# Kernel optimization log

Measured on AMD Instinct MI355X. Metric: run time of the kernel, lower is better.

Reference implementation:

```python
import jax, jax.numpy as jnp
import numpy as np

B, BS, M, D = 64, 8, 512, 256  # b = bs * neg_sample_num, neg_sample_num = 8
NEG_FILL = -1e10


def setup_inputs() -> dict:
    key = jax.random.key(0)
    ks = jax.random.split(key, 7)
    x = jax.random.normal(ks[0], (B, M, D), jnp.float32)
    y = jax.random.normal(ks[1], (BS, M, D), jnp.float32)
    mask_x = jax.random.randint(ks[2], (B, M), 0, 2).astype(bool).at[:, 0].set(True)
    mask_y = jax.random.randint(ks[3], (BS, M), 0, 2).astype(bool).at[:, 0].set(True)
    scale = 1.0 / np.sqrt(D)
    Wq = jax.random.normal(ks[4], (D, D), jnp.float32) * scale  # torch Linear weight [out,in]
    Wk = jax.random.normal(ks[5], (D, D), jnp.float32) * scale
    Wv = jax.random.normal(ks[6], (D, D), jnp.float32) * scale
    return {"x": x, "y": y, "mask_x": mask_x, "mask_y": mask_y, "Wq": Wq, "Wk": Wk, "Wv": Wv}


def reference(x, y, mask_x, mask_y, Wq, Wk, Wv):
    # Projections (torch Linear: x @ W.T, no bias)
    Qx, Kx, Vx = x @ Wq.T, x @ Wk.T, x @ Wv.T
    Qy, Ky, Vy = y @ Wq.T, y @ Wk.T, y @ Wv.T
    b, m, d = Qx.shape
    bs = Ky.shape[0]
    neg = b // bs  # neg_sample_num branch (bs != b)

    scores_x = jnp.einsum('bid,bjd->bij', Qx, Kx)   # [b,m,m]
    scores_y = jnp.einsum('bid,bjd->bij', Qy, Ky)   # [bs,m,m]
    # Q_x grouped as [bs, neg, m, d] then transposed to [neg, bs, m, d];
    # K_y is tiled over neg (pure broadcast), so contract directly against [bs,m,d].
    Qx_e = Qx.reshape(bs, neg, m, d).swapaxes(0, 1)  # [neg,bs,m,d]
    scores_xy = jnp.einsum('nsid,sjd->nsij', Qx_e, Ky)  # [neg,bs,m,m]

    mx = mask_x[:, :, None]  # [b,m,1]
    my = mask_y[:, :, None]  # [bs,m,1]
    scores_x = jnp.where(mx & mx.swapaxes(1, 2), scores_x, NEG_FILL)
    scores_y = jnp.where(my & my.swapaxes(1, 2), scores_y, NEG_FILL)

    mask_xy = mask_x.reshape(bs, neg, m, 1).swapaxes(0, 1) & mask_y[None, :, None, :]  # [neg,bs,m,m]
    scores_xy = jnp.where(mask_xy, scores_xy, NEG_FILL)

    # y_len[n, s] = sum(mask_y[s]) for every n (repeat/view/sum/transpose in torch)
    y_len = jnp.broadcast_to(jnp.sum(mask_y.astype(jnp.int32), axis=1)[None, :], (neg, bs))

    probs_x = jax.nn.softmax(scores_x, axis=-1)
    probs_y = jax.nn.softmax(scores_y, axis=-1)
    probs_xy = jax.nn.softmax(scores_xy, axis=-1)

    ctx_x = jnp.einsum('bij,bjd->bid', probs_x, Vx)
    ctx_y = jnp.einsum('bij,bjd->bid', probs_y, Vy)
    return (ctx_x, ctx_y, scores_x, scores_y, probs_xy, mask_xy, y_len)
```

## Files before the change

### kernel.cpp

```cpp
#include <hip/hip_runtime.h>
#include <cstdint>

#define NEG_FILL_F (-10000000000.0f)
constexpr int BB     = 64;
constexpr int BS_    = 8;
constexpr int MM     = 512;
constexpr int DD     = 256;
constexpr int ROWS_X = BB * MM;
constexpr int ROWS_Y = BS_ * MM;
constexpr int ROWS_ALL = ROWS_X + ROWS_Y;
constexpr int KS     = 512;

typedef __attribute__((ext_vector_type(8))) short short8;
typedef __attribute__((ext_vector_type(4))) float f32x4;

__device__ inline unsigned short rne_bf16(float f) {
    unsigned int u = __float_as_uint(f);
    u = (u + 0x7FFFu + ((u >> 16) & 1u)) >> 16;
    return (unsigned short)u;
}
__device__ inline float bf2f(unsigned short h) {
    return __uint_as_float(((unsigned int)h) << 16);
}

__device__ inline f32x4 mfma16(short8 a, short8 b, f32x4 c) {
    return __builtin_amdgcn_mfma_f32_16x16x32_bf16(a, b, c, 0, 0, 0);
}

__device__ inline void gld16(const unsigned short* g, unsigned short* l) {
    __builtin_amdgcn_global_load_lds(
        (const __attribute__((address_space(1))) unsigned int*)g,
        (__attribute__((address_space(3))) unsigned int*)l, 16, 0, 0);
}

__device__ inline int awin32(int w) { return (((w >> 3) == 1) ? 256 : 0) + (w & 7) * 32; }
__device__ inline int bwin32(int w) { return (((w >> 3) == 2) ? 256 : 0) + (w & 7) * 32; }

__device__ inline void stage32(unsigned short* dstbase,
                               const unsigned short* __restrict__ src,
                               int srccol, int wave, int lane)
{
    #pragma unroll
    for (int s4 = 0; s4 < 2; ++s4) {
        const int c   = s4 * 256 + wave * 64 + lane;
        const int r   = c >> 2;
        const int cin = (c & 3) ^ (r & 3);
        gld16(src + (size_t)r * KS + srccol + cin * 8,
              dstbase + (size_t)(s4 * 256 + wave * 64) * 8);
    }
}

__device__ inline void frag4_x32(const unsigned short (*T)[32], int rbase,
                                 int lid, int quad, short8 f[4])
{
    const int q = quad ^ (lid & 3);
    #pragma unroll
    for (int i = 0; i < 4; ++i)
        f[i] = *(const short8*)&T[rbase + i * 16 + lid][q * 8];
}

__global__ __launch_bounds__(256) void convw_kernel(
    const float* __restrict__ Wq, const float* __restrict__ Wk,
    const float* __restrict__ Wv, unsigned short* __restrict__ Wb)
{
    const int g  = blockIdx.x * 256 + threadIdx.x;
    const int e  = g * 8;
    const int zi = e >> 16;
    const int off = e & 65535;
    const int row = off >> 8, k0 = off & 255;
    const float* W = (zi == 0) ? Wq : (zi == 1 ? Wk : Wv);
    float4 v0 = *(const float4*)(W + off);
    float4 v1 = *(const float4*)(W + off + 4);
    const float fv[8] = {v0.x, v0.y, v0.z, v0.w, v1.x, v1.y, v1.z, v1.w};
    short8 hh, ll;
    #pragma unroll
    for (int i = 0; i < 8; ++i) {
        unsigned short h = rne_bf16(fv[i]);
        hh[i] = (short)h;
        ll[i] = (short)rne_bf16(fv[i] - bf2f(h));
    }
    unsigned short* dst = Wb + (size_t)zi * 131072 + (size_t)row * KS;
    *(short8*)(dst + k0)       = hh;
    *(short8*)(dst + 256 + k0) = ll;
}

__global__ __launch_bounds__(256) void convx_kernel(
    const float* __restrict__ x, const float* __restrict__ y,
    unsigned short* __restrict__ xs)
{
    const int g   = blockIdx.x * 256 + threadIdx.x;
    const int row = g >> 5;
    const int off = (g & 31) * 8;
    const float* src = (row < ROWS_X) ? (x + (size_t)row * DD)
                                      : (y + (size_t)(row - ROWS_X) * DD);
    float4 v0 = *(const float4*)(src + off);
    float4 v1 = *(const float4*)(src + off + 4);
    const float fv[8] = {v0.x, v0.y, v0.z, v0.w, v1.x, v1.y, v1.z, v1.w};
    short8 hh, ll;
    #pragma unroll
    for (int i = 0; i < 8; ++i) {
        unsigned short h = rne_bf16(fv[i]);
        hh[i] = (short)h;
        ll[i] = (short)rne_bf16(fv[i] - bf2f(h));
    }
    unsigned short* dst = xs + (size_t)row * KS;
    *(short8*)(dst + off)       = hh;
    *(short8*)(dst + 256 + off) = ll;
}

__global__ __launch_bounds__(256) void proj_kernel(
    const unsigned short* __restrict__ xs,
    const unsigned short* __restrict__ Wb,
    unsigned short* __restrict__ Qa, unsigned short* __restrict__ Kb,
    unsigned short* __restrict__ Vt)
{
    const int xcd = blockIdx.x & 7, idx = blockIdx.x >> 3;
    const int lin = xcd * 216 + idx;
    const int bx  = lin / 6;
    const int rem = lin - bx * 6;
    const int z    = rem >> 1;
    const int row0 = bx * 128;
    const int col0 = (rem & 1) * 128;
    const unsigned short* Asrc = xs + (size_t)row0 * KS;
    const unsigned short* Bsrc = Wb + (size_t)z * 131072 + (size_t)col0 * KS;

    __shared__ unsigned short Ab[2][128][32];
    __shared__ unsigned short Bb[2][128][32];

    const int t = threadIdx.x;
    const int wave = t >> 6, lane = t & 63, quad = lane >> 4, lid = lane & 15;
    const int wrow = (wave & 1) * 64, wcol = (wave >> 1) * 64;

    f32x4 acc[4][4];
    #pragma unroll
    for (int i = 0; i < 4; ++i)
        #pragma unroll
        for (int j = 0; j < 4; ++j) acc[i][j] = (f32x4){0.f, 0.f, 0.f, 0.f};

    stage32(&Ab[0][0][0], Asrc, awin32(0), wave, lane);
    stage32(&Bb[0][0][0], Bsrc, bwin32(0), wave, lane);
    __syncthreads();
    int cur = 0;
    for (int w = 0; w < 23; ++w) {
        stage32(&Ab[cur ^ 1][0][0], Asrc, awin32(w + 1), wave, lane);
        stage32(&Bb[cur ^ 1][0][0], Bsrc, bwin32(w + 1), wave, lane);
        short8 af[4], bf_[4];
        frag4_x32(Ab[cur], wrow, lid, quad, af);
        frag4_x32(Bb[cur], wcol, lid, quad, bf_);
        #pragma unroll
        for (int i = 0; i < 4; ++i)
            #pragma unroll
            for (int j = 0; j < 4; ++j)
                acc[i][j] = mfma16(af[i], bf_[j], acc[i][j]);
        __syncthreads();
        cur ^= 1;
    }
    {
        short8 af[4], bf_[4];
        frag4_x32(Ab[cur], wrow, lid, quad, af);
        frag4_x32(Bb[cur], wcol, lid, quad, bf_);
        #pragma unroll
        for (int i = 0; i < 4; ++i)
            #pragma unroll
            for (int j = 0; j < 4; ++j)
                acc[i][j] = mfma16(af[i], bf_[j], acc[i][j]);
    }

    if (z == 2) {
        #pragma unroll
        for (int i = 0; i < 4; ++i) {
            const int rg = row0 + wrow + i * 16 + quad * 4;
            const int b  = rg >> 9;
            const int j  = rg & 511;
            #pragma unroll
            for (int jt = 0; jt < 4; ++jt) {
                const int col = col0 + wcol + jt * 16 + lid;
                *(ushort4*)(Vt + (size_t)b * DD * MM + (size_t)col * MM + j) =
                    make_ushort4(rne_bf16(acc[i][jt][0]), rne_bf16(acc[i][jt][1]),
                                 rne_bf16(acc[i][jt][2]), rne_bf16(acc[i][jt][3]));
            }
        }
    } else {
        unsigned short* dst = (z == 0) ? Qa : Kb;
        #pragma unroll
        for (int i = 0; i < 4; ++i) {
            const int rg = row0 + wrow + i * 16 + quad * 4;
            #pragma unroll
            for (int r = 0; r < 4; ++r) {
                unsigned short* rowp = dst + (size_t)(rg + r) * KS;
                #pragma unroll
                for (int jt = 0; jt < 4; ++jt) {
                    const int col = col0 + wcol + jt * 16 + lid;
                    const float v = acc[i][jt][r];
                    unsigned short h = rne_bf16(v);
                    rowp[col]       = h;
                    rowp[256 + col] = rne_bf16(v - bf2f(h));
                }
            }
        }
    }
}

__global__ __launch_bounds__(256, 2) void scores_self_kernel(
    const unsigned short* __restrict__ Qa,
    const unsigned short* __restrict__ Kb,
    const int* __restrict__ mask_x, const int* __restrict__ mask_y,
    float* __restrict__ Sbase, unsigned short* __restrict__ P,
    float* __restrict__ inv_all)
{
    const int xcd = blockIdx.x & 7, idx = blockIdx.x >> 3;
    const int lin = xcd * 72 + idx;
    const int z    = lin >> 3;
    const int brow = (lin & 7) * 64;
    const unsigned short* Asrc = Qa + (size_t)(z * MM + brow) * KS;
    const unsigned short* Bsrc = Kb + (size_t)z * MM * KS;
    const int* msk = (z < 64) ? (mask_x + z * MM) : (mask_y + (z - 64) * MM);
    float* S = Sbase + (size_t)z * MM * MM;

    __shared__ unsigned short Ab[2][64][32];
    __shared__ unsigned short Bb[2][512][32];
    __shared__ float pm4[64][4], ps4[64][4], smx[64];

    const int t = threadIdx.x;
    const int wave = t >> 6, lane = t & 63, quad = lane >> 4, lid = lane & 15;
    const int wcol = wave * 128;

    f32x4 acc[4][8];
    #pragma unroll
    for (int i = 0; i < 4; ++i)
        #pragma unroll
        for (int j = 0; j < 8; ++j) acc[i][j] = (f32x4){0.f, 0.f, 0.f, 0.f};

    auto stage = [&](int buf, int w) {
        {
            const int r = t >> 2, cin = (t & 3) ^ (r & 3);
            gld16(Asrc + (size_t)r * KS + awin32(w) + cin * 8,
                  &Ab[buf][0][0] + (size_t)(wave * 64) * 8);
        }
        const int bw = bwin32(w);
        #pragma unroll
        for (int k = 0; k < 8; ++k) {
            const int c = k * 256 + t;
            const int r = c >> 2, cin = (c & 3) ^ (r & 3);
            gld16(Bsrc + (size_t)r * KS + bw + cin * 8,
                  &Bb[buf][0][0] + (size_t)(k * 256 + wave * 64) * 8);
        }
    };
    auto comp = [&](int buf) {
        short8 af[4], bv[8];
        frag4_x32(Ab[buf], 0, lid, quad, af);
        frag4_x32(Bb[buf], wcol, lid, quad, bv);
        frag4_x32(Bb[buf], wcol + 64, lid, quad, bv + 4);
        #pragma unroll
        for (int i = 0; i < 4; ++i)
            #pragma unroll
            for (int j = 0; j < 8; ++j)
                acc[i][j] = mfma16(af[i], bv[j], acc[i][j]);
    };

    stage(0, 0);
    __syncthreads();
    int cur = 0;
    for (int w = 0; w < 23; ++w) {
        stage(cur ^ 1, w + 1);
        comp(cur);
        __syncthreads();
        cur ^= 1;
    }
    comp(cur);

    int mcol[8];
    #pragma unroll
    for (int j = 0; j < 8; ++j) mcol[j] = msk[wcol + j * 16 + lid];

    #pragma unroll
    for (int i = 0; i < 4; ++i) {
        #pragma unroll
        for (int r = 0; r < 4; ++r) {
            const int rl = i * 16 + quad * 4 + r;
            const bool mr = (msk[brow + rl] != 0);
            float* Srow = S + (size_t)(brow + rl) * MM;
            float vv[8];
            float mt = -3.4e38f;
            #pragma unroll
            for (int j = 0; j < 8; ++j) {
                const int col = wcol + j * 16 + lid;
                const bool valid = mr && (mcol[j] != 0);
                vv[j] = valid ? acc[i][j][r] : NEG_FILL_F;
                Srow[col] = vv[j];
                mt = fmaxf(mt, vv[j]);
            }
            #pragma unroll
            for (int o = 1; o < 16; o <<= 1) mt = fmaxf(mt, __shfl_xor(mt, o));
            float se = 0.f;
            #pragma unroll
            for (int j = 0; j < 8; ++j) se += __expf(vv[j] - mt);
            #pragma unroll
            for (int o = 1; o < 16; o <<= 1) se += __shfl_xor(se, o);
            if (lid == 0) { pm4[rl][wave] = mt; ps4[rl][wave] = se; }
        }
    }
    __syncthreads();
    if (t < 64) {
        const float m = fmaxf(fmaxf(pm4[t][0], pm4[t][1]),
                              fmaxf(pm4[t][2], pm4[t][3]));
        float s = 0.f;
        #pragma unroll
        for (int c = 0; c < 4; ++c) s += ps4[t][c] * __expf(pm4[t][c] - m);
        smx[t] = m;
        inv_all[z * MM + brow + t] = 1.0f / s;
    }
    __syncthreads();
    #pragma unroll
    for (int i = 0; i < 4; ++i) {
        #pragma unroll
        for (int r = 0; r < 4; ++r) {
            const int rl = i * 16 + quad * 4 + r;
            const bool mr = (msk[brow + rl] != 0);
            const float m = smx[rl];
            unsigned short* Prow = P + (size_t)(z * MM + brow + rl) * KS;
            #pragma unroll
            for (int j = 0; j < 8; ++j) {
                const int col = wcol + j * 16 + lid;
                const bool valid = mr && (mcol[j] != 0);
                const float v = valid ? acc[i][j][r] : NEG_FILL_F;
                Prow[col] = rne_bf16(__expf(v - m));
            }
        }
    }
}

__global__ __launch_bounds__(256, 2) void scores_xy_kernel(
    const unsigned short* __restrict__ Qa, const unsigned short* __restrict__ Kb,
    const int* __restrict__ mask_x, const int* __restrict__ mask_y,
    float* __restrict__ Prb, float* __restrict__ Mb)
{
    const int xcd = blockIdx.x & 7, idx = blockIdx.x >> 3;
    const int lin = xcd * 64 + idx;
    const int zz = lin >> 3;
    const int brow = (lin & 7) * 64;
    const int s = zz >> 3, n = zz & 7;
    const int zo = n * 8 + s;
    const int bq = s * 8 + n;
    const int bk = s;
    const unsigned short* Asrc = Qa + (size_t)(bq * MM + brow) * KS;
    const unsigned short* Bsrc = Kb + (size_t)(ROWS_X + bk * MM) * KS;
    const int* mq = mask_x + bq * MM;
    const int* mk = mask_y + bk * MM;
    float* Pl = Prb + (size_t)zo * MM * MM;
    float* Ml = Mb  + (size_t)zo * MM * MM;

    __shared__ unsigned short Ab[2][64][32];
    __shared__ unsigned short Bb[2][512][32];
    __shared__ float pm4[64][4], ps4[64][4], smx[64], sin[64];

    const int t = threadIdx.x;
    const int wave = t >> 6, lane = t & 63, quad = lane >> 4, lid = lane & 15;
    const int wcol = wave * 128;

    f32x4 acc[4][8];
    #pragma unroll
    for (int i = 0; i < 4; ++i)
        #pragma unroll
        for (int j = 0; j < 8; ++j) acc[i][j] = (f32x4){0.f, 0.f, 0.f, 0.f};

    auto stage = [&](int buf, int w) {
        {
            const int r = t >> 2, cin = (t & 3) ^ (r & 3);
            gld16(Asrc + (size_t)r * KS + w * 32 + cin * 8,
                  &Ab[buf][0][0] + (size_t)(wave * 64) * 8);
        }
        #pragma unroll
        for (int k = 0; k < 8; ++k) {
            const int c = k * 256 + t;
            const int r = c >> 2, cin = (c & 3) ^ (r & 3);
            gld16(Bsrc + (size_t)r * KS + w * 32 + cin * 8,
                  &Bb[buf][0][0] + (size_t)(k * 256 + wave * 64) * 8);
        }
    };
    auto comp = [&](int buf) {
        short8 af[4], bv[8];
        frag4_x32(Ab[buf], 0, lid, quad, af);
        frag4_x32(Bb[buf], wcol, lid, quad, bv);
        frag4_x32(Bb[buf], wcol + 64, lid, quad, bv + 4);
        #pragma unroll
        for (int i = 0; i < 4; ++i)
            #pragma unroll
            for (int j = 0; j < 8; ++j)
                acc[i][j] = mfma16(af[i], bv[j], acc[i][j]);
    };

    stage(0, 0);
    __syncthreads();
    int cur = 0;
    for (int w = 0; w < 7; ++w) {
        stage(cur ^ 1, w + 1);
        comp(cur);
        __syncthreads();
        cur ^= 1;
    }
    comp(cur);

    int mcol[8];
    #pragma unroll
    for (int j = 0; j < 8; ++j) mcol[j] = mk[wcol + j * 16 + lid];

    #pragma unroll
    for (int i = 0; i < 4; ++i) {
        #pragma unroll
        for (int r = 0; r < 4; ++r) {
            const int rl = i * 16 + quad * 4 + r;
            const bool mr = (mq[brow + rl] != 0);
            float* Mrow = Ml + (size_t)(brow + rl) * MM;
            float vv[8];
            float mt = -3.4e38f;
            #pragma unroll
            for (int j = 0; j < 8; ++j) {
                const int col = wcol + j * 16 + lid;
                const bool valid = mr && (mcol[j] != 0);
                vv[j] = valid ? acc[i][j][r] : NEG_FILL_F;
                Mrow[col] = valid ? 1.0f : 0.0f;
                mt = fmaxf(mt, vv[j]);
            }
            #pragma unroll
            for (int o = 1; o < 16; o <<= 1) mt = fmaxf(mt, __shfl_xor(mt, o));
            float se = 0.f;
            #pragma unroll
            for (int j = 0; j < 8; ++j) se += __expf(vv[j] - mt);
            #pragma unroll
            for (int o = 1; o < 16; o <<= 1) se += __shfl_xor(se, o);
            if (lid == 0) { pm4[rl][wave] = mt; ps4[rl][wave] = se; }
        }
    }
    __syncthreads();
    if (t < 64) {
        const float m = fmaxf(fmaxf(pm4[t][0], pm4[t][1]),
                              fmaxf(pm4[t][2], pm4[t][3]));
        float ssum = 0.f;
        #pragma unroll
        for (int c = 0; c < 4; ++c) ssum += ps4[t][c] * __expf(pm4[t][c] - m);
        smx[t] = m;
        sin[t] = 1.0f / ssum;
    }
    __syncthreads();
    #pragma unroll
    for (int i = 0; i < 4; ++i) {
        #pragma unroll
        for (int r = 0; r < 4; ++r) {
            const int rl = i * 16 + quad * 4 + r;
            const bool mr = (mq[brow + rl] != 0);
            const float m = smx[rl], iv = sin[rl];
            float* Prow = Pl + (size_t)(brow + rl) * MM;
            #pragma unroll
            for (int j = 0; j < 8; ++j) {
                const int col = wcol + j * 16 + lid;
                const bool valid = mr && (mcol[j] != 0);
                const float v = valid ? acc[i][j][r] : NEG_FILL_F;
                Prow[col] = __expf(v - m) * iv;
            }
        }
    }
}

__global__ __launch_bounds__(256) void ctx_kernel(
    const unsigned short* __restrict__ P, const float* __restrict__ inv_all,
    const unsigned short* __restrict__ Vt_base, float* __restrict__ Obase)
{
    const int xcd = blockIdx.x & 7, idx = blockIdx.x >> 3;
    const int lin = xcd * 72 + idx;
    const int b    = lin >> 3;
    const int brow = (lin & 7) * 64;
    const unsigned short* Psrc = P + (size_t)(b * MM + brow) * KS;
    const unsigned short* Vt   = Vt_base + (size_t)b * DD * MM;
    float*                O    = Obase + (size_t)b * MM * DD;
    const float*          iv   = inv_all + b * MM + brow;

    __shared__ unsigned short Ab[2][64][32];
    __shared__ unsigned short Bb[2][256][32];

    const int t = threadIdx.x;
    const int wave = t >> 6, lane = t & 63, quad = lane >> 4, lid = lane & 15;
    const int wcol = wave * 64;

    f32x4 acc[4][4];
    #pragma unroll
    for (int i = 0; i < 4; ++i)
        #pragma unroll
        for (int j = 0; j < 4; ++j) acc[i][j] = (f32x4){0.f, 0.f, 0.f, 0.f};

    auto stage = [&](int buf, int w) {
        {
            const int r = t >> 2, cin = (t & 3) ^ (r & 3);
            gld16(Psrc + (size_t)r * KS + w * 32 + cin * 8,
                  &Ab[buf][0][0] + (size_t)(wave * 64) * 8);
        }
        #pragma unroll
        for (int k = 0; k < 4; ++k) {
            const int c = k * 256 + t;
            const int r = c >> 2, cin = (c & 3) ^ (r & 3);
            gld16(Vt + (size_t)r * MM + w * 32 + cin * 8,
                  &Bb[buf][0][0] + (size_t)(k * 256 + wave * 64) * 8);
        }
    };
    auto comp = [&](int buf) {
        short8 af[4], bf_[4];
        frag4_x32(Ab[buf], 0, lid, quad, af);
        frag4_x32(Bb[buf], wcol, lid, quad, bf_);
        #pragma unroll
        for (int i = 0; i < 4; ++i)
            #pragma unroll
            for (int j = 0; j < 4; ++j)
                acc[i][j] = mfma16(af[i], bf_[j], acc[i][j]);
    };

    stage(0, 0);
    __syncthreads();
    int cur = 0;
    for (int w = 0; w < 15; ++w) {
        stage(cur ^ 1, w + 1);
        comp(cur);
        __syncthreads();
        cur ^= 1;
    }
    comp(cur);

    #pragma unroll
    for (int i = 0; i < 4; ++i) {
        const int rl0 = i * 16 + quad * 4;
        float inv[4];
        #pragma unroll
        for (int r = 0; r < 4; ++r) inv[r] = iv[rl0 + r];
        #pragma unroll
        for (int jt = 0; jt < 4; ++jt) {
            const int col = wcol + jt * 16 + lid;
            #pragma unroll
            for (int r = 0; r < 4; ++r)
                O[(size_t)(brow + rl0 + r) * DD + col] = acc[i][jt][r] * inv[r];
        }
    }
}

__global__ void ylen_kernel(const int* __restrict__ mask_y, float* __restrict__ out)
{
    const int s = blockIdx.x;
    const int lane = threadIdx.x;
    int c = 0;
    #pragma unroll
    for (int k = 0; k < 8; ++k) c += (mask_y[s * MM + k * 64 + lane] != 0);
    #pragma unroll
    for (int off = 32; off; off >>= 1) c += __shfl_xor(c, off);
    if (lane < 8) out[lane * 8 + s] = (float)c;
}

extern "C" void kernel_launch(void* const* d_in, const int* in_sizes, int n_in,
                              void* d_out, int out_size, void* d_ws, size_t ws_size,
                              hipStream_t stream)
{
    const float* x      = (const float*)d_in[0];
    const float* y      = (const float*)d_in[1];
    const int*   mask_x = (const int*)d_in[2];
    const int*   mask_y = (const int*)d_in[3];
    const float* Wq     = (const float*)d_in[4];
    const float* Wk     = (const float*)d_in[5];
    const float* Wv     = (const float*)d_in[6];
    float* out = (float*)d_out;

    unsigned short* Wb = (unsigned short*)d_ws;
    unsigned short* xs = Wb + 393216;
    unsigned short* Qa = xs + 18874368;
    unsigned short* Kb = Qa + 18874368;
    unsigned short* Vt = Kb + 18874368;
    float* inv_all = (float*)(Vt + 9437184);

    float* out_ctx   = out;
    float* out_sx    = out + 9437184;
    float* out_pxy   = out + 28311552;
    float* out_mxy   = out + 45088768;
    float* out_ylen  = out + 61865984;

    unsigned short* P = (unsigned short*)out_pxy;

    convw_kernel<<<96, 256, 0, stream>>>(Wq, Wk, Wv, Wb);
    convx_kernel<<<4608, 256, 0, stream>>>(x, y, xs);
    ylen_kernel<<<8, 64, 0, stream>>>(mask_y, out_ylen);

    proj_kernel<<<1728, 256, 0, stream>>>(xs, Wb, Qa, Kb, Vt);

    scores_self_kernel<<<576, 256, 0, stream>>>(
        Qa, Kb, mask_x, mask_y, out_sx, P, inv_all);

    ctx_kernel<<<576, 256, 0, stream>>>(P, inv_all, Vt, out_ctx);

    scores_xy_kernel<<<512, 256, 0, stream>>>(
        Qa, Kb, mask_x, mask_y, out_pxy, out_mxy);
}
```

Measured before the change: 465.1 us.

## Fuse self-attention scores and context into one kernel with P kept in LDS

Merges the scores_self and ctx kernels into a single self_attn kernel. The unnormalized bf16 probabilities stay in shared memory and are multiplied by V directly instead of round-tripping through global memory, and the separate inv_all buffer goes away. Block size doubles to 512 threads with 8 waves splitting columns, and a shared-memory union reuses the QK staging area for P and V tiles. The aim is to save one kernel launch and the global write and read of P, at the cost of more LDS per block and fewer MFMAs per wave.

```diff
diff --git a/kernel.cpp b/kernel.cpp
--- a/kernel.cpp
+++ b/kernel.cpp
@@ -201,12 +201,12 @@
     }
 }
 
-__global__ __launch_bounds__(256, 2) void scores_self_kernel(
+__global__ __launch_bounds__(512) void self_attn_kernel(
     const unsigned short* __restrict__ Qa,
     const unsigned short* __restrict__ Kb,
     const int* __restrict__ mask_x, const int* __restrict__ mask_y,
-    float* __restrict__ Sbase, unsigned short* __restrict__ P,
-    float* __restrict__ inv_all)
+    const unsigned short* __restrict__ Vt_base,
+    float* __restrict__ Sbase, float* __restrict__ Obase)
 {
     const int xcd = blockIdx.x & 7, idx = blockIdx.x >> 3;
     const int lin = xcd * 72 + idx;
@@ -214,64 +214,70 @@
     const int brow = (lin & 7) * 64;
     const unsigned short* Asrc = Qa + (size_t)(z * MM + brow) * KS;
     const unsigned short* Bsrc = Kb + (size_t)z * MM * KS;
+    const unsigned short* Vt   = Vt_base + (size_t)z * DD * MM;
     const int* msk = (z < 64) ? (mask_x + z * MM) : (mask_y + (z - 64) * MM);
     float* S = Sbase + (size_t)z * MM * MM;
-
-    __shared__ unsigned short Ab[2][64][32];
-    __shared__ unsigned short Bb[2][512][32];
-    __shared__ float pm4[64][4], ps4[64][4], smx[64];
+    float* O = Obase + (size_t)z * MM * DD;
+
+    __shared__ union {
+        struct { unsigned short A[2][64][32];
+                 unsigned short B[2][512][32]; } qk;
+        struct { unsigned short P[64][520];
+                 unsigned short V[2][256][32]; } pv;
+    } sh;
+    __shared__ float pm8[64][8], ps8[64][8], smx[64], sin_[64];
 
     const int t = threadIdx.x;
     const int wave = t >> 6, lane = t & 63, quad = lane >> 4, lid = lane & 15;
-    const int wcol = wave * 128;
-
-    f32x4 acc[4][8];
+    const int wcol = wave * 64;
+
+    f32x4 acc[4][4];
     #pragma unroll
     for (int i = 0; i < 4; ++i)
         #pragma unroll
-        for (int j = 0; j < 8; ++j) acc[i][j] = (f32x4){0.f, 0.f, 0.f, 0.f};
-
-    auto stage = [&](int buf, int w) {
-        {
-            const int r = t >> 2, cin = (t & 3) ^ (r & 3);
+        for (int j = 0; j < 4; ++j) acc[i][j] = (f32x4){0.f, 0.f, 0.f, 0.f};
+
+    auto stageQK = [&](int buf, int w) {
+        if (wave < 4) {
+            const int c = t;
+            const int r = c >> 2, cin = (c & 3) ^ (r & 3);
             gld16(Asrc + (size_t)r * KS + awin32(w) + cin * 8,
-                  &Ab[buf][0][0] + (size_t)(wave * 64) * 8);
+                  &sh.qk.A[buf][0][0] + (size_t)(wave * 64) * 8);
         }
         const int bw = bwin32(w);
         #pragma unroll
-        for (int k = 0; k < 8; ++k) {
-            const int c = k * 256 + t;
+        for (int k = 0; k < 4; ++k) {
+            const int c = k * 512 + t;
             const int r = c >> 2, cin = (c & 3) ^ (r & 3);
             gld16(Bsrc + (size_t)r * KS + bw + cin * 8,
-                  &Bb[buf][0][0] + (size_t)(k * 256 + wave * 64) * 8);
+                  &sh.qk.B[buf][0][0] + (size_t)(k * 512 + wave * 64) * 8);
         }
     };
-    auto comp = [&](int buf) {
-        short8 af[4], bv[8];
-        frag4_x32(Ab[buf], 0, lid, quad, af);
-        frag4_x32(Bb[buf], wcol, lid, quad, bv);
-        frag4_x32(Bb[buf], wcol + 64, lid, quad, bv + 4);
+    auto compQK = [&](int buf) {
+        short8 af[4], bf_[4];
+        frag4_x32(sh.qk.A[buf], 0, lid, quad, af);
+        frag4_x32(sh.qk.B[buf], wcol, lid, quad, bf_);
         #pragma unroll
         for (int i = 0; i < 4; ++i)
             #pragma unroll
-            for (int j = 0; j < 8; ++j)
-                acc[i][j] = mfma16(af[i], bv[j], acc[i][j]);
+            for (int j = 0; j < 4; ++j)
+                acc[i][j] = mfma16(af[i], bf_[j], acc[i][j]);
     };
 
-    stage(0, 0);
+    stageQK(0, 0);
     __syncthreads();
     int cur = 0;
     for (int w = 0; w < 23; ++w) {
-        stage(cur ^ 1, w + 1);
-        comp(cur);
+        stageQK(cur ^ 1, w + 1);
+        compQK(cur);
         __syncthreads();
         cur ^= 1;
     }
-    comp(cur);
-
-    int mcol[8];
-    #pragma unroll
-    for (int j = 0; j < 8; ++j) mcol[j] = msk[wcol + j * 16 + lid];
+    compQK(cur);
+
+    int mcol[4];
+    #pragma unroll
+    for (int j = 0; j < 4; ++j) mcol[j] = msk[wcol + j * 16 + lid];
 
     #pragma unroll
     for (int i = 0; i < 4; ++i) {
@@ -280,10 +286,10 @@
             const int rl = i * 16 + quad * 4 + r;
             const bool mr = (msk[brow + rl] != 0);
             float* Srow = S + (size_t)(brow + rl) * MM;
-            float vv[8];
+            float vv[4];
             float mt = -3.4e38f;
             #pragma unroll
-            for (int j = 0; j < 8; ++j) {
+            for (int j = 0; j < 4; ++j) {
                 const int col = wcol + j * 16 + lid;
                 const bool valid = mr && (mcol[j] != 0);
                 vv[j] = valid ? acc[i][j][r] : NEG_FILL_F;
@@ -294,23 +300,35 @@
             for (int o = 1; o < 16; o <<= 1) mt = fmaxf(mt, __shfl_xor(mt, o));
             float se = 0.f;
             #pragma unroll
-            for (int j = 0; j < 8; ++j) se += __expf(vv[j] - mt);
+            for (int j = 0; j < 4; ++j) se += __expf(vv[j] - mt);
             #pragma unroll
             for (int o = 1; o < 16; o <<= 1) se += __shfl_xor(se, o);
-            if (lid == 0) { pm4[rl][wave] = mt; ps4[rl][wave] = se; }
+            if (lid == 0) { pm8[rl][wave] = mt; ps8[rl][wave] = se; }
         }
     }
     __syncthreads();
     if (t < 64) {
-        const float m = fmaxf(fmaxf(pm4[t][0], pm4[t][1]),
-                              fmaxf(pm4[t][2], pm4[t][3]));
+        float m = -3.4e38f;
+        #pragma unroll
+        for (int c = 0; c < 8; ++c) m = fmaxf(m, pm8[t][c]);
         float s = 0.f;
         #pragma unroll
-        for (int c = 0; c < 4; ++c) s += ps4[t][c] * __expf(pm4[t][c] - m);
+        for (int c = 0; c < 8; ++c) s += ps8[t][c] * __expf(pm8[t][c] - m);
         smx[t] = m;
-        inv_all[z * MM + brow + t] = 1.0f / s;
-    }
-    __syncthreads();
+        sin_[t] = 1.0f / s;
+    }
+    __syncthreads();
+
+    auto stageV = [&](int buf, int w) {
+        #pragma unroll
+        for (int k = 0; k < 2; ++k) {
+            const int c = k * 512 + t;
+            const int r = c >> 2, cin = (c & 3) ^ (r & 3);
+            gld16(Vt + (size_t)r * MM + w * 32 + cin * 8,
+                  &sh.pv.V[buf][0][0] + (size_t)(k * 512 + wave * 64) * 8);
+        }
+    };
+    stageV(0, 0);
     #pragma unroll
     for (int i = 0; i < 4; ++i) {
         #pragma unroll
@@ -318,14 +336,61 @@
             const int rl = i * 16 + quad * 4 + r;
             const bool mr = (msk[brow + rl] != 0);
             const float m = smx[rl];
-            unsigned short* Prow = P + (size_t)(z * MM + brow + rl) * KS;
-            #pragma unroll
-            for (int j = 0; j < 8; ++j) {
+            #pragma unroll
+            for (int j = 0; j < 4; ++j) {
                 const int col = wcol + j * 16 + lid;
                 const bool valid = mr && (mcol[j] != 0);
                 const float v = valid ? acc[i][j][r] : NEG_FILL_F;
-                Prow[col] = rne_bf16(__expf(v - m));
+                sh.pv.P[rl][col] = rne_bf16(__expf(v - m));
             }
+        }
+    }
+    __syncthreads();
+
+    f32x4 acc2[4][2];
+    #pragma unroll
+    for (int i = 0; i < 4; ++i)
+        #pragma unroll
+        for (int j = 0; j < 2; ++j) acc2[i][j] = (f32x4){0.f, 0.f, 0.f, 0.f};
+    const int pcol = wave * 32;
+
+    auto compPV = [&](int buf, int w) {
+        short8 af[4], bf_[2];
+        #pragma unroll
+        for (int i = 0; i < 4; ++i)
+            af[i] = *(const short8*)&sh.pv.P[i * 16 + lid][w * 32 + quad * 8];
+        const int q = quad ^ (lid & 3);
+        #pragma unroll
+        for (int j = 0; j < 2; ++j)
+            bf_[j] = *(const short8*)&sh.pv.V[buf][pcol + j * 16 + lid][q * 8];
+        #pragma unroll
+        for (int i = 0; i < 4; ++i)
+            #pragma unroll
+            for (int j = 0; j < 2; ++j)
+                acc2[i][j] = mfma16(af[i], bf_[j], acc2[i][j]);
+    };
+
+    int cv = 0;
+    for (int w = 0; w < 15; ++w) {
+        stageV(cv ^ 1, w + 1);
+        compPV(cv, w);
+        __syncthreads();
+        cv ^= 1;
+    }
+    compPV(cv, 15);
+
+    #pragma unroll
+    for (int i = 0; i < 4; ++i) {
+        const int rl0 = i * 16 + quad * 4;
+        float inv[4];
+        #pragma unroll
+        for (int r = 0; r < 4; ++r) inv[r] = sin_[rl0 + r];
+        #pragma unroll
+        for (int j = 0; j < 2; ++j) {
+            const int col = pcol + j * 16 + lid;
+            #pragma unroll
+            for (int r = 0; r < 4; ++r)
+                O[(size_t)(brow + rl0 + r) * DD + col] = acc2[i][j][r] * inv[r];
         }
     }
 }
@@ -352,7 +417,7 @@
 
     __shared__ unsigned short Ab[2][64][32];
     __shared__ unsigned short Bb[2][512][32];
-    __shared__ float pm4[64][4], ps4[64][4], smx[64], sin[64];
+    __shared__ float pm4[64][4], ps4[64][4], smx[64], sin_[64];
 
     const int t = threadIdx.x;
     const int wave = t >> 6, lane = t & 63, quad = lane >> 4, lid = lane & 15;
@@ -440,7 +505,7 @@
         #pragma unroll
         for (int c = 0; c < 4; ++c) ssum += ps4[t][c] * __expf(pm4[t][c] - m);
         smx[t] = m;
-        sin[t] = 1.0f / ssum;
+        sin_[t] = 1.0f / ssum;
     }
     __syncthreads();
     #pragma unroll
@@ -449,7 +514,7 @@
         for (int r = 0; r < 4; ++r) {
             const int rl = i * 16 + quad * 4 + r;
             const bool mr = (mq[brow + rl] != 0);
-            const float m = smx[rl], iv = sin[rl];
+            const float m = smx[rl], iv = sin_[rl];
             float* Prow = Pl + (size_t)(brow + rl) * MM;
             #pragma unroll
             for (int j = 0; j < 8; ++j) {
@@ -458,84 +523,6 @@
                 const float v = valid ? acc[i][j][r] : NEG_FILL_F;
                 Prow[col] = __expf(v - m) * iv;
             }
-        }
-    }
-}
-
-__global__ __launch_bounds__(256) void ctx_kernel(
-    const unsigned short* __restrict__ P, const float* __restrict__ inv_all,
-    const unsigned short* __restrict__ Vt_base, float* __restrict__ Obase)
-{
-    const int xcd = blockIdx.x & 7, idx = blockIdx.x >> 3;
-    const int lin = xcd * 72 + idx;
-    const int b    = lin >> 3;
-    const int brow = (lin & 7) * 64;
-    const unsigned short* Psrc = P + (size_t)(b * MM + brow) * KS;
-    const unsigned short* Vt   = Vt_base + (size_t)b * DD * MM;
-    float*                O    = Obase + (size_t)b * MM * DD;
-    const float*          iv   = inv_all + b * MM + brow;
-
-    __shared__ unsigned short Ab[2][64][32];
-    __shared__ unsigned short Bb[2][256][32];
-
-    const int t = threadIdx.x;
-    const int wave = t >> 6, lane = t & 63, quad = lane >> 4, lid = lane & 15;
-    const int wcol = wave * 64;
-
-    f32x4 acc[4][4];
-    #pragma unroll
-    for (int i = 0; i < 4; ++i)
-        #pragma unroll
-        for (int j = 0; j < 4; ++j) acc[i][j] = (f32x4){0.f, 0.f, 0.f, 0.f};
-
-    auto stage = [&](int buf, int w) {
-        {
-            const int r = t >> 2, cin = (t & 3) ^ (r & 3);
-            gld16(Psrc + (size_t)r * KS + w * 32 + cin * 8,
-                  &Ab[buf][0][0] + (size_t)(wave * 64) * 8);
-        }
-        #pragma unroll
-        for (int k = 0; k < 4; ++k) {
-            const int c = k * 256 + t;
-            const int r = c >> 2, cin = (c & 3) ^ (r & 3);
-            gld16(Vt + (size_t)r * MM + w * 32 + cin * 8,
-                  &Bb[buf][0][0] + (size_t)(k * 256 + wave * 64) * 8);
-        }
-    };
-    auto comp = [&](int buf) {
-        short8 af[4], bf_[4];
-        frag4_x32(Ab[buf], 0, lid, quad, af);
-        frag4_x32(Bb[buf], wcol, lid, quad, bf_);
-        #pragma unroll
-        for (int i = 0; i < 4; ++i)
-            #pragma unroll
-            for (int j = 0; j < 4; ++j)
-                acc[i][j] = mfma16(af[i], bf_[j], acc[i][j]);
-    };
-
-    stage(0, 0);
-    __syncthreads();
-    int cur = 0;
-    for (int w = 0; w < 15; ++w) {
-        stage(cur ^ 1, w + 1);
-        comp(cur);
-        __syncthreads();
-        cur ^= 1;
-    }
-    comp(cur);
-
-    #pragma unroll
-    for (int i = 0; i < 4; ++i) {
-        const int rl0 = i * 16 + quad * 4;
-        float inv[4];
-        #pragma unroll
-        for (int r = 0; r < 4; ++r) inv[r] = iv[rl0 + r];
-        #pragma unroll
-        for (int jt = 0; jt < 4; ++jt) {
-            const int col = wcol + jt * 16 + lid;
-            #pragma unroll
-            for (int r = 0; r < 4; ++r)
-                O[(size_t)(brow + rl0 + r) * DD + col] = acc[i][jt][r] * inv[r];
         }
     }
 }
@@ -570,7 +557,6 @@
     unsigned short* Qa = xs + 18874368;
     unsigned short* Kb = Qa + 18874368;
     unsigned short* Vt = Kb + 18874368;
-    float* inv_all = (float*)(Vt + 9437184);
 
     float* out_ctx   = out;
     float* out_sx    = out + 9437184;
@@ -578,18 +564,14 @@
     float* out_mxy   = out + 45088768;
     float* out_ylen  = out + 61865984;
 
-    unsigned short* P = (unsigned short*)out_pxy;
-
     convw_kernel<<<96, 256, 0, stream>>>(Wq, Wk, Wv, Wb);
     convx_kernel<<<4608, 256, 0, stream>>>(x, y, xs);
     ylen_kernel<<<8, 64, 0, stream>>>(mask_y, out_ylen);
 
     proj_kernel<<<1728, 256, 0, stream>>>(xs, Wb, Qa, Kb, Vt);
 
-    scores_self_kernel<<<576, 256, 0, stream>>>(
-        Qa, Kb, mask_x, mask_y, out_sx, P, inv_all);
-
-    ctx_kernel<<<576, 256, 0, stream>>>(P, inv_all, Vt, out_ctx);
+    self_attn_kernel<<<576, 512, 0, stream>>>(
+        Qa, Kb, mask_x, mask_y, Vt, out_sx, out_ctx);
 
     scores_xy_kernel<<<512, 256, 0, stream>>>(
         Qa, Kb, mask_x, mask_y, out_pxy, out_mxy);
```

New measurement: 472.8 us. Within noise of the previous version (+1.7%).

## Merge prep kernels and switch proj/ctx GEMMs to single-buffered 64-wide K tiles

Applied to the files above, without the earlier changes.

Folds the weight conversion, input conversion and y_len kernels into one launch to cut launch overhead. The projection and context GEMMs drop double-buffered 32-wide K tiles for single-buffered 64-wide tiles with an 8-way XOR swizzle, halving the number of barrier iterations. In exchange, global loads no longer overlap with MFMA work inside a block, so the kernels rely on other resident blocks to hide latency. A shared array is also renamed from sin to sin_ to avoid clashing with the math function.

```diff
diff --git a/kernel.cpp b/kernel.cpp
--- a/kernel.cpp
+++ b/kernel.cpp
@@ -33,79 +33,104 @@
         (__attribute__((address_space(3))) unsigned int*)l, 16, 0, 0);
 }
 
+__device__ inline int awin64(int w) { return (((w >> 2) == 1) ? 256 : 0) + (w & 3) * 64; }
+__device__ inline int bwin64(int w) { return (((w >> 2) == 2) ? 256 : 0) + (w & 3) * 64; }
+
+__device__ inline void stage64(unsigned short* dstbase,
+                               const unsigned short* __restrict__ src,
+                               int srccol, int wave, int lane)
+{
+    #pragma unroll
+    for (int s4 = 0; s4 < 4; ++s4) {
+        const int c   = s4 * 256 + wave * 64 + lane;
+        const int r   = c >> 3;
+        const int cin = (c & 7) ^ (r & 7);
+        gld16(src + (size_t)r * KS + srccol + cin * 8,
+              dstbase + (size_t)(s4 * 256 + wave * 64) * 8);
+    }
+}
+
+__device__ inline void frag4_x64(const unsigned short (*T)[64], int rbase,
+                                 int lid, int c0, short8 f[4])
+{
+    const int q = c0 ^ (lid & 7);
+    #pragma unroll
+    for (int i = 0; i < 4; ++i)
+        f[i] = *(const short8*)&T[rbase + i * 16 + lid][q * 8];
+}
+
+__device__ inline void frag4_x32(const unsigned short (*T)[32], int rbase,
+                                 int lid, int quad, short8 f[4])
+{
+    const int q = quad ^ (lid & 3);
+    #pragma unroll
+    for (int i = 0; i < 4; ++i)
+        f[i] = *(const short8*)&T[rbase + i * 16 + lid][q * 8];
+}
+
 __device__ inline int awin32(int w) { return (((w >> 3) == 1) ? 256 : 0) + (w & 7) * 32; }
 __device__ inline int bwin32(int w) { return (((w >> 3) == 2) ? 256 : 0) + (w & 7) * 32; }
 
-__device__ inline void stage32(unsigned short* dstbase,
-                               const unsigned short* __restrict__ src,
-                               int srccol, int wave, int lane)
-{
-    #pragma unroll
-    for (int s4 = 0; s4 < 2; ++s4) {
-        const int c   = s4 * 256 + wave * 64 + lane;
-        const int r   = c >> 2;
-        const int cin = (c & 3) ^ (r & 3);
-        gld16(src + (size_t)r * KS + srccol + cin * 8,
-              dstbase + (size_t)(s4 * 256 + wave * 64) * 8);
-    }
-}
-
-__device__ inline void frag4_x32(const unsigned short (*T)[32], int rbase,
-                                 int lid, int quad, short8 f[4])
-{
-    const int q = quad ^ (lid & 3);
-    #pragma unroll
-    for (int i = 0; i < 4; ++i)
-        f[i] = *(const short8*)&T[rbase + i * 16 + lid][q * 8];
-}
-
-__global__ __launch_bounds__(256) void convw_kernel(
+__global__ __launch_bounds__(256) void prep_kernel(
+    const float* __restrict__ x, const float* __restrict__ y,
     const float* __restrict__ Wq, const float* __restrict__ Wk,
-    const float* __restrict__ Wv, unsigned short* __restrict__ Wb)
-{
-    const int g  = blockIdx.x * 256 + threadIdx.x;
-    const int e  = g * 8;
-    const int zi = e >> 16;
-    const int off = e & 65535;
-    const int row = off >> 8, k0 = off & 255;
-    const float* W = (zi == 0) ? Wq : (zi == 1 ? Wk : Wv);
-    float4 v0 = *(const float4*)(W + off);
-    float4 v1 = *(const float4*)(W + off + 4);
-    const float fv[8] = {v0.x, v0.y, v0.z, v0.w, v1.x, v1.y, v1.z, v1.w};
-    short8 hh, ll;
-    #pragma unroll
-    for (int i = 0; i < 8; ++i) {
-        unsigned short h = rne_bf16(fv[i]);
-        hh[i] = (short)h;
-        ll[i] = (short)rne_bf16(fv[i] - bf2f(h));
-    }
-    unsigned short* dst = Wb + (size_t)zi * 131072 + (size_t)row * KS;
-    *(short8*)(dst + k0)       = hh;
-    *(short8*)(dst + 256 + k0) = ll;
-}
-
-__global__ __launch_bounds__(256) void convx_kernel(
-    const float* __restrict__ x, const float* __restrict__ y,
-    unsigned short* __restrict__ xs)
-{
-    const int g   = blockIdx.x * 256 + threadIdx.x;
-    const int row = g >> 5;
-    const int off = (g & 31) * 8;
-    const float* src = (row < ROWS_X) ? (x + (size_t)row * DD)
-                                      : (y + (size_t)(row - ROWS_X) * DD);
-    float4 v0 = *(const float4*)(src + off);
-    float4 v1 = *(const float4*)(src + off + 4);
-    const float fv[8] = {v0.x, v0.y, v0.z, v0.w, v1.x, v1.y, v1.z, v1.w};
-    short8 hh, ll;
-    #pragma unroll
-    for (int i = 0; i < 8; ++i) {
-        unsigned short h = rne_bf16(fv[i]);
-        hh[i] = (short)h;
-        ll[i] = (short)rne_bf16(fv[i] - bf2f(h));
-    }
-    unsigned short* dst = xs + (size_t)row * KS;
-    *(short8*)(dst + off)       = hh;
-    *(short8*)(dst + 256 + off) = ll;
+    const float* __restrict__ Wv, const int* __restrict__ mask_y,
+    unsigned short* __restrict__ xs, unsigned short* __restrict__ Wb,
+    float* __restrict__ ylen_out)
+{
+    const int bid = blockIdx.x;
+    const int t   = threadIdx.x;
+    if (bid < 4608) {
+        const int g   = bid * 256 + t;
+        const int row = g >> 5;
+        const int off = (g & 31) * 8;
+        const float* src = (row < ROWS_X) ? (x + (size_t)row * DD)
+                                          : (y + (size_t)(row - ROWS_X) * DD);
+        float4 v0 = *(const float4*)(src + off);
+        float4 v1 = *(const float4*)(src + off + 4);
+        const float fv[8] = {v0.x, v0.y, v0.z, v0.w, v1.x, v1.y, v1.z, v1.w};
+        short8 hh, ll;
+        #pragma unroll
+        for (int i = 0; i < 8; ++i) {
+            unsigned short h = rne_bf16(fv[i]);
+            hh[i] = (short)h;
+            ll[i] = (short)rne_bf16(fv[i] - bf2f(h));
+        }
+        unsigned short* dst = xs + (size_t)row * KS;
+        *(short8*)(dst + off)       = hh;
+        *(short8*)(dst + 256 + off) = ll;
+    } else if (bid < 4704) {
+        const int g  = (bid - 4608) * 256 + t;
+        const int e  = g * 8;
+        const int zi = e >> 16;
+        const int off = e & 65535;
+        const int row = off >> 8, k0 = off & 255;
+        const float* W = (zi == 0) ? Wq : (zi == 1 ? Wk : Wv);
+        float4 v0 = *(const float4*)(W + off);
+        float4 v1 = *(const float4*)(W + off + 4);
+        const float fv[8] = {v0.x, v0.y, v0.z, v0.w, v1.x, v1.y, v1.z, v1.w};
+        short8 hh, ll;
+        #pragma unroll
+        for (int i = 0; i < 8; ++i) {
+            unsigned short h = rne_bf16(fv[i]);
+            hh[i] = (short)h;
+            ll[i] = (short)rne_bf16(fv[i] - bf2f(h));
+        }
+        unsigned short* dst = Wb + (size_t)zi * 131072 + (size_t)row * KS;
+        *(short8*)(dst + k0)       = hh;
+        *(short8*)(dst + 256 + k0) = ll;
+    } else {
+        if (t < 64) {
+            const int s = bid - 4704;
+            int c = 0;
+            #pragma unroll
+            for (int k = 0; k < 8; ++k)
+                c += (mask_y[s * MM + k * 64 + t] != 0);
+            #pragma unroll
+            for (int off = 32; off; off >>= 1) c += __shfl_xor(c, off);
+            if (t < 8) ylen_out[t * 8 + s] = (float)c;
+        }
+    }
 }
 
 __global__ __launch_bounds__(256) void proj_kernel(
@@ -124,8 +149,8 @@
     const unsigned short* Asrc = xs + (size_t)row0 * KS;
     const unsigned short* Bsrc = Wb + (size_t)z * 131072 + (size_t)col0 * KS;
 
-    __shared__ unsigned short Ab[2][128][32];
-    __shared__ unsigned short Bb[2][128][32];
+    __shared__ unsigned short Ab[128][64];
+    __shared__ unsigned short Bb[128][64];
 
     const int t = threadIdx.x;
     const int wave = t >> 6, lane = t & 63, quad = lane >> 4, lid = lane & 15;
@@ -137,33 +162,23 @@
         #pragma unroll
         for (int j = 0; j < 4; ++j) acc[i][j] = (f32x4){0.f, 0.f, 0.f, 0.f};
 
-    stage32(&Ab[0][0][0], Asrc, awin32(0), wave, lane);
-    stage32(&Bb[0][0][0], Bsrc, bwin32(0), wave, lane);
-    __syncthreads();
-    int cur = 0;
-    for (int w = 0; w < 23; ++w) {
-        stage32(&Ab[cur ^ 1][0][0], Asrc, awin32(w + 1), wave, lane);
-        stage32(&Bb[cur ^ 1][0][0], Bsrc, bwin32(w + 1), wave, lane);
-        short8 af[4], bf_[4];
-        frag4_x32(Ab[cur], wrow, lid, quad, af);
-        frag4_x32(Bb[cur], wcol, lid, quad, bf_);
-        #pragma unroll
-        for (int i = 0; i < 4; ++i)
-            #pragma unroll
-            for (int j = 0; j < 4; ++j)
-                acc[i][j] = mfma16(af[i], bf_[j], acc[i][j]);
+    for (int w = 0; w < 12; ++w) {
+        stage64(&Ab[0][0], Asrc, awin64(w), wave, lane);
+        stage64(&Bb[0][0], Bsrc, bwin64(w), wave, lane);
         __syncthreads();
-        cur ^= 1;
-    }
-    {
-        short8 af[4], bf_[4];
-        frag4_x32(Ab[cur], wrow, lid, quad, af);
-        frag4_x32(Bb[cur], wcol, lid, quad, bf_);
-        #pragma unroll
-        for (int i = 0; i < 4; ++i)
-            #pragma unroll
-            for (int j = 0; j < 4; ++j)
-                acc[i][j] = mfma16(af[i], bf_[j], acc[i][j]);
+        #pragma unroll
+        for (int kk = 0; kk < 64; kk += 32) {
+            const int c0 = (kk >> 3) + quad;
+            short8 af[4], bf_[4];
+            frag4_x64(Ab, wrow, lid, c0, af);
+            frag4_x64(Bb, wcol, lid, c0, bf_);
+            #pragma unroll
+            for (int i = 0; i < 4; ++i)
+                #pragma unroll
+                for (int j = 0; j < 4; ++j)
+                    acc[i][j] = mfma16(af[i], bf_[j], acc[i][j]);
+        }
+        __syncthreads();
     }
 
     if (z == 2) {
@@ -352,7 +367,7 @@
 
     __shared__ unsigned short Ab[2][64][32];
     __shared__ unsigned short Bb[2][512][32];
-    __shared__ float pm4[64][4], ps4[64][4], smx[64], sin[64];
+    __shared__ float pm4[64][4], ps4[64][4], smx[64], sin_[64];
 
     const int t = threadIdx.x;
     const int wave = t >> 6, lane = t & 63, quad = lane >> 4, lid = lane & 15;
@@ -440,7 +455,7 @@
         #pragma unroll
         for (int c = 0; c < 4; ++c) ssum += ps4[t][c] * __expf(pm4[t][c] - m);
         smx[t] = m;
-        sin[t] = 1.0f / ssum;
+        sin_[t] = 1.0f / ssum;
     }
     __syncthreads();
     #pragma unroll
@@ -449,7 +464,7 @@
         for (int r = 0; r < 4; ++r) {
             const int rl = i * 16 + quad * 4 + r;
             const bool mr = (mq[brow + rl] != 0);
-            const float m = smx[rl], iv = sin[rl];
+            const float m = smx[rl], iv = sin_[rl];
             float* Prow = Pl + (size_t)(brow + rl) * MM;
             #pragma unroll
             for (int j = 0; j < 8; ++j) {
@@ -475,8 +490,8 @@
     float*                O    = Obase + (size_t)b * MM * DD;
     const float*          iv   = inv_all + b * MM + brow;
 
-    __shared__ unsigned short Ab[2][64][32];
-    __shared__ unsigned short Bb[2][256][32];
+    __shared__ unsigned short Ab[64][64];
+    __shared__ unsigned short Bb[256][64];
 
     const int t = threadIdx.x;
     const int wave = t >> 6, lane = t & 63, quad = lane >> 4, lid = lane & 15;
@@ -488,41 +503,36 @@
         #pragma unroll
         for (int j = 0; j < 4; ++j) acc[i][j] = (f32x4){0.f, 0.f, 0.f, 0.f};
 
-    auto stage = [&](int buf, int w) {
-        {
-            const int r = t >> 2, cin = (t & 3) ^ (r & 3);
-            gld16(Psrc + (size_t)r * KS + w * 32 + cin * 8,
-                  &Ab[buf][0][0] + (size_t)(wave * 64) * 8);
-        }
-        #pragma unroll
-        for (int k = 0; k < 4; ++k) {
-            const int c = k * 256 + t;
-            const int r = c >> 2, cin = (c & 3) ^ (r & 3);
-            gld16(Vt + (size_t)r * MM + w * 32 + cin * 8,
-                  &Bb[buf][0][0] + (size_t)(k * 256 + wave * 64) * 8);
-        }
-    };
-    auto comp = [&](int buf) {
-        short8 af[4], bf_[4];
-        frag4_x32(Ab[buf], 0, lid, quad, af);
-        frag4_x32(Bb[buf], wcol, lid, quad, bf_);
-        #pragma unroll
-        for (int i = 0; i < 4; ++i)
-            #pragma unroll
-            for (int j = 0; j < 4; ++j)
-                acc[i][j] = mfma16(af[i], bf_[j], acc[i][j]);
-    };
-
-    stage(0, 0);
-    __syncthreads();
-    int cur = 0;
-    for (int w = 0; w < 15; ++w) {
-        stage(cur ^ 1, w + 1);
-        comp(cur);
+    for (int w = 0; w < 8; ++w) {
+        #pragma unroll
+        for (int s4 = 0; s4 < 2; ++s4) {
+            const int c = s4 * 256 + wave * 64 + lane;
+            const int r = c >> 3, cin = (c & 7) ^ (r & 7);
+            gld16(Psrc + (size_t)r * KS + w * 64 + cin * 8,
+                  &Ab[0][0] + (size_t)(s4 * 256 + wave * 64) * 8);
+        }
+        #pragma unroll
+        for (int k = 0; k < 8; ++k) {
+            const int c = k * 256 + wave * 64 + lane;
+            const int r = c >> 3, cin = (c & 7) ^ (r & 7);
+            gld16(Vt + (size_t)r * MM + w * 64 + cin * 8,
+                  &Bb[0][0] + (size_t)(k * 256 + wave * 64) * 8);
+        }
         __syncthreads();
-        cur ^= 1;
-    }
-    comp(cur);
+        #pragma unroll
+        for (int kk = 0; kk < 64; kk += 32) {
+            const int c0 = (kk >> 3) + quad;
+            short8 af[4], bf_[4];
+            frag4_x64(Ab, 0, lid, c0, af);
+            frag4_x64(Bb, wcol, lid, c0, bf_);
+            #pragma unroll
+            for (int i = 0; i < 4; ++i)
+                #pragma unroll
+                for (int j = 0; j < 4; ++j)
+                    acc[i][j] = mfma16(af[i], bf_[j], acc[i][j]);
+        }
+        __syncthreads();
+    }
 
     #pragma unroll
     for (int i = 0; i < 4; ++i) {
@@ -538,18 +548,6 @@
                 O[(size_t)(brow + rl0 + r) * DD + col] = acc[i][jt][r] * inv[r];
         }
     }
-}
-
-__global__ void ylen_kernel(const int* __restrict__ mask_y, float* __restrict__ out)
-{
-    const int s = blockIdx.x;
-    const int lane = threadIdx.x;
-    int c = 0;
-    #pragma unroll
-    for (int k = 0; k < 8; ++k) c += (mask_y[s * MM + k * 64 + lane] != 0);
-    #pragma unroll
-    for (int off = 32; off; off >>= 1) c += __shfl_xor(c, off);
-    if (lane < 8) out[lane * 8 + s] = (float)c;
 }
 
 extern "C" void kernel_launch(void* const* d_in, const int* in_sizes, int n_in,
@@ -580,9 +578,8 @@
 
     unsigned short* P = (unsigned short*)out_pxy;
 
-    convw_kernel<<<96, 256, 0, stream>>>(Wq, Wk, Wv, Wb);
-    convx_kernel<<<4608, 256, 0, stream>>>(x, y, xs);
-    ylen_kernel<<<8, 64, 0, stream>>>(mask_y, out_ylen);
+    prep_kernel<<<4712, 256, 0, stream>>>(x, y, Wq, Wk, Wv, mask_y,
+                                          xs, Wb, out_ylen);
 
     proj_kernel<<<1728, 256, 0, stream>>>(xs, Wb, Qa, Kb, Vt);
 
```

Result: no change. 462.5 us (-0.6%).
